# Optimization experiments

Hardware: AMD Instinct MI355X
Metric: run time of the kernel (lower is better)

## Reference

```python
import jax, jax.numpy as jnp
import numpy as np

N_NODES = 100000
N_EDGES = 1600000
IN_DIM = 128
OUT_DIM = 32


def setup_inputs() -> dict:
    key = jax.random.key(0)
    k1, k2, k3, k4, k5 = jax.random.split(key, 5)
    x = jax.random.normal(k1, (N_NODES, IN_DIM), dtype=jnp.float32)
    adj_rows = jax.random.randint(k2, (N_EDGES,), 0, N_NODES, dtype=jnp.int32)
    adj_cols = jax.random.randint(k3, (N_EDGES,), 0, N_NODES, dtype=jnp.int32)
    adj_vals = jax.random.uniform(k4, (N_EDGES,), dtype=jnp.float32)
    # kaiming-uniform-like init for weight, zeros for bias (as in init_parameters)
    bound = float(np.sqrt(6.0 / IN_DIM))
    weight = jax.random.uniform(k5, (IN_DIM, OUT_DIM), minval=-bound, maxval=bound, dtype=jnp.float32)
    bias = jnp.zeros((OUT_DIM,), dtype=jnp.float32)
    return {"x": x, "adj_rows": adj_rows, "adj_cols": adj_cols,
            "adj_vals": adj_vals, "weight": weight, "bias": bias}


def reference(x, adj_rows, adj_cols, adj_vals, weight, bias):
    # support = X @ W  -> [N, OUT_DIM]
    support = x @ weight
    # output = A_sparse @ support  (COO SpMM via gather + segment-sum)
    gathered = adj_vals[:, None] * support[adj_cols]          # [E, OUT_DIM]
    output = jax.ops.segment_sum(gathered, adj_rows, num_segments=N_NODES)
    return output + bias
```

## Files before the change

kernel.cpp:

```cpp
#include <hip/hip_runtime.h>

#define N_NODES 100000
#define N_EDGES 1600000
#define IN_DIM 128
#define OUT_DIM 32

typedef _Float16 h2 __attribute__((ext_vector_type(2)));

__global__ __launch_bounds__(256) void gemm_support(
    const float* __restrict__ x, const float* __restrict__ w,
    _Float16* __restrict__ support, unsigned* __restrict__ out_h_words) {
  __shared__ float ws[IN_DIM][OUT_DIM];
  __shared__ float xs[8][IN_DIM];
  const int tid = threadIdx.x;

  {
    const float4* w4 = (const float4*)w;
    float4* ws4 = (float4*)&ws[0][0];
    for (int i = tid; i < IN_DIM * OUT_DIM / 4; i += 256) ws4[i] = w4[i];
  }
  const int row0 = blockIdx.x * 8;
  {
    const float4* x4 = (const float4*)(x + (long long)row0 * IN_DIM);
    float4* xs4 = (float4*)&xs[0][0];
    xs4[tid] = x4[tid];
  }
  __syncthreads();

  const int r = tid >> 5;
  const int c = tid & 31;
  float acc = 0.f;
#pragma unroll
  for (int k = 0; k < IN_DIM; ++k)
    acc = fmaf(xs[r][k], ws[k][c], acc);
  support[(long long)(row0 + r) * OUT_DIM + c] = (_Float16)acc;

  const int g = blockIdx.x * 256 + tid;
  if (g < N_NODES * OUT_DIM / 2) out_h_words[g] = 0u;
}

__device__ __forceinline__ void pk_atomic_add_h2(h2* p, h2 v) {
#if __has_builtin(__builtin_amdgcn_global_atomic_fadd_v2f16)
  __builtin_amdgcn_global_atomic_fadd_v2f16(
      (__attribute__((address_space(1))) h2*)p, v);
#else
  unsigned* pu = (unsigned*)p;
  unsigned old = *pu;
  while (true) {
    h2 cur = __builtin_bit_cast(h2, old);
    h2 nv = cur + v;
    unsigned n = __builtin_bit_cast(unsigned, nv);
    unsigned r = atomicCAS(pu, old, n);
    if (r == old) break;
    old = r;
  }
#endif
}

__global__ __launch_bounds__(256) void scatter_h2(
    const int* __restrict__ rows, const int* __restrict__ cols,
    const float* __restrict__ vals, const _Float16* __restrict__ support,
    h2* __restrict__ out_h) {
  const long long gid = (long long)blockIdx.x * 256 + threadIdx.x;
  if (gid >= (long long)N_EDGES * 16) return;
  const int e = (int)(gid >> 4);
  const int l = (int)(gid & 15);
  const int r = rows[e];
  const int c = cols[e];
  const float v = vals[e];
  const h2 s = *(const h2*)(support + (long long)c * OUT_DIM + 2 * l);
  h2 inc = { (_Float16)(v * (float)s[0]), (_Float16)(v * (float)s[1]) };
  pk_atomic_add_h2(out_h + (long long)r * 16 + l, inc);
}

__global__ __launch_bounds__(256) void finalize_h(
    const h2* __restrict__ out_h, const float* __restrict__ bias,
    float* __restrict__ out) {
  const int i = blockIdx.x * 256 + threadIdx.x;
  if (i >= N_NODES * OUT_DIM / 8) return;
  const h2* src = out_h + i * 4;
  float4 a, b;
  h2 p0 = src[0], p1 = src[1], p2 = src[2], p3 = src[3];
  const int d0 = (i * 8) & 31;
  a.x = (float)p0[0] + bias[d0 + 0];
  a.y = (float)p0[1] + bias[d0 + 1];
  a.z = (float)p1[0] + bias[d0 + 2];
  a.w = (float)p1[1] + bias[d0 + 3];
  b.x = (float)p2[0] + bias[d0 + 4];
  b.y = (float)p2[1] + bias[d0 + 5];
  b.z = (float)p3[0] + bias[d0 + 6];
  b.w = (float)p3[1] + bias[d0 + 7];
  float4* dst = (float4*)(out + (long long)i * 8);
  dst[0] = a;
  dst[1] = b;
}

extern "C" void kernel_launch(void* const* d_in, const int* in_sizes, int n_in,
                              void* d_out, int out_size, void* d_ws, size_t ws_size,
                              hipStream_t stream) {
  const float* x        = (const float*)d_in[0];
  const int*   adj_rows = (const int*)d_in[1];
  const int*   adj_cols = (const int*)d_in[2];
  const float* adj_vals = (const float*)d_in[3];
  const float* weight   = (const float*)d_in[4];
  const float* bias     = (const float*)d_in[5];
  float* out = (float*)d_out;

  char* wsp = (char*)d_ws;
  _Float16* support = (_Float16*)wsp;
  h2* out_h = (h2*)(wsp + 6400000);

  gemm_support<<<N_NODES / 8, 256, 0, stream>>>(x, weight, support,
                                                (unsigned*)out_h);
  {
    const long long total = (long long)N_EDGES * 16;
    scatter_h2<<<(int)((total + 255) / 256), 256, 0, stream>>>(
        adj_rows, adj_cols, adj_vals, support, out_h);
  }
  {
    const int total = N_NODES * OUT_DIM / 8;
    finalize_h<<<(total + 255) / 256, 256, 0, stream>>>(out_h, bias, out);
  }
}
```

Measured before the change: 134.1 us.

## Register-tile support GEMM with 64-row blocks and vectorized zeroing

The support GEMM now processes 64 rows per block instead of 8, with each thread computing a 2x4 output tile from padded, transposed shared-memory weights and float4 LDS reads. This cuts the per-block weight reload and raises FMA-to-LDS-load ratio. Output zeroing uses uint4 stores across the now-fewer blocks. The scatter kernel drops its bounds check, since the edge count divides evenly by the block size.

```diff
diff --git a/kernel.cpp b/kernel.cpp
--- a/kernel.cpp
+++ b/kernel.cpp
@@ -6,37 +6,68 @@
 #define OUT_DIM 32
 
 typedef _Float16 h2 __attribute__((ext_vector_type(2)));
+typedef _Float16 h4 __attribute__((ext_vector_type(4)));
+
+#define FMA4(acc, s, wv)                  \
+  acc.x = fmaf(s, wv.x, acc.x);           \
+  acc.y = fmaf(s, wv.y, acc.y);           \
+  acc.z = fmaf(s, wv.z, acc.z);           \
+  acc.w = fmaf(s, wv.w, acc.w)
 
 __global__ __launch_bounds__(256) void gemm_support(
     const float* __restrict__ x, const float* __restrict__ w,
-    _Float16* __restrict__ support, unsigned* __restrict__ out_h_words) {
-  __shared__ float ws[IN_DIM][OUT_DIM];
-  __shared__ float xs[8][IN_DIM];
-  const int tid = threadIdx.x;
+    _Float16* __restrict__ support, uint4* __restrict__ out_h_vec) {
+  __shared__ float xs[64][132];
+  __shared__ float w4[8][129][4];
+  const int t = threadIdx.x;
+  const long long row0 = (long long)blockIdx.x * 64;
 
-  {
-    const float4* w4 = (const float4*)w;
-    float4* ws4 = (float4*)&ws[0][0];
-    for (int i = tid; i < IN_DIM * OUT_DIM / 4; i += 256) ws4[i] = w4[i];
+  for (int i = t; i < IN_DIM * OUT_DIM; i += 256) {
+    const int k = i >> 5, c = i & 31;
+    w4[c >> 2][k][c & 3] = w[i];
   }
-  const int row0 = blockIdx.x * 8;
-  {
-    const float4* x4 = (const float4*)(x + (long long)row0 * IN_DIM);
-    float4* xs4 = (float4*)&xs[0][0];
-    xs4[tid] = x4[tid];
+  for (int j = t; j < 64 * (IN_DIM / 4); j += 256) {
+    const int r = j >> 5;
+    const int f = j & 31;
+    const long long row = row0 + r;
+    float4 v = (row < N_NODES) ? ((const float4*)x)[row * (IN_DIM / 4) + f]
+                               : make_float4(0.f, 0.f, 0.f, 0.f);
+    *(float4*)&xs[r][f * 4] = v;
   }
   __syncthreads();
 
-  const int r = tid >> 5;
-  const int c = tid & 31;
-  float acc = 0.f;
+  const int rr = t >> 3;
+  const int cc = t & 7;
+  float4 a0 = make_float4(0.f, 0.f, 0.f, 0.f);
+  float4 a1 = make_float4(0.f, 0.f, 0.f, 0.f);
 #pragma unroll
-  for (int k = 0; k < IN_DIM; ++k)
-    acc = fmaf(xs[r][k], ws[k][c], acc);
-  support[(long long)(row0 + r) * OUT_DIM + c] = (_Float16)acc;
+  for (int k4 = 0; k4 < IN_DIM / 4; ++k4) {
+    const int k = k4 * 4;
+    const float4 xv0 = *(const float4*)&xs[2 * rr][k];
+    const float4 xv1 = *(const float4*)&xs[2 * rr + 1][k];
+    const float4 w0 = *(const float4*)&w4[cc][k][0];
+    const float4 w1 = *(const float4*)&w4[cc][k + 1][0];
+    const float4 w2 = *(const float4*)&w4[cc][k + 2][0];
+    const float4 w3 = *(const float4*)&w4[cc][k + 3][0];
+    FMA4(a0, xv0.x, w0); FMA4(a0, xv0.y, w1);
+    FMA4(a0, xv0.z, w2); FMA4(a0, xv0.w, w3);
+    FMA4(a1, xv1.x, w0); FMA4(a1, xv1.y, w1);
+    FMA4(a1, xv1.z, w2); FMA4(a1, xv1.w, w3);
+  }
 
-  const int g = blockIdx.x * 256 + tid;
-  if (g < N_NODES * OUT_DIM / 2) out_h_words[g] = 0u;
+  const long long r0 = row0 + 2 * rr;
+  if (r0 < N_NODES) {
+    h4 o = { (_Float16)a0.x, (_Float16)a0.y, (_Float16)a0.z, (_Float16)a0.w };
+    *(h4*)(support + r0 * OUT_DIM + 4 * cc) = o;
+  }
+  const long long r1 = r0 + 1;
+  if (r1 < N_NODES) {
+    h4 o = { (_Float16)a1.x, (_Float16)a1.y, (_Float16)a1.z, (_Float16)a1.w };
+    *(h4*)(support + r1 * OUT_DIM + 4 * cc) = o;
+  }
+
+  const int g = blockIdx.x * 256 + t;
+  if (g < N_NODES * OUT_DIM * 2 / 16) out_h_vec[g] = make_uint4(0, 0, 0, 0);
 }
 
 __device__ __forceinline__ void pk_atomic_add_h2(h2* p, h2 v) {
@@ -62,7 +93,6 @@
     const float* __restrict__ vals, const _Float16* __restrict__ support,
     h2* __restrict__ out_h) {
   const long long gid = (long long)blockIdx.x * 256 + threadIdx.x;
-  if (gid >= (long long)N_EDGES * 16) return;
   const int e = (int)(gid >> 4);
   const int l = (int)(gid & 15);
   const int r = rows[e];
@@ -110,11 +140,11 @@
   _Float16* support = (_Float16*)wsp;
   h2* out_h = (h2*)(wsp + 6400000);
 
-  gemm_support<<<N_NODES / 8, 256, 0, stream>>>(x, weight, support,
-                                                (unsigned*)out_h);
+  gemm_support<<<(N_NODES + 63) / 64, 256, 0, stream>>>(
+      x, weight, support, (uint4*)out_h);
   {
     const long long total = (long long)N_EDGES * 16;
-    scatter_h2<<<(int)((total + 255) / 256), 256, 0, stream>>>(
+    scatter_h2<<<(int)(total / 256), 256, 0, stream>>>(
         adj_rows, adj_cols, adj_vals, support, out_h);
   }
   {
```

Measured after the change: 118.7 us (median of 2 runs). 11.5% less time.
